# Kernel tuning notes

Measured on AMD Instinct MI355X. Metric: run time of the kernel, lower is better.

## Reference

```python
import jax, jax.numpy as jnp
import numpy as np

N = 50000        # total nodes (disjoint batch of graphs)
E = 800000       # total edges
F_IN = 8         # node feature dim
S = 6            # edge feature dim
H = 20           # ECC kernel-network hidden size (hidden_states)
N_OUT = 20       # ECC output channels (n_out=hidden_states)
G = 32           # GCN channels
D1 = 16          # first dense
N_GRAPHS = 512   # graphs in batch


def setup_inputs() -> dict:
    key = jax.random.key(0)
    ks = jax.random.split(key, 24)
    r = lambda k, sh, s: jax.random.normal(k, sh, dtype=jnp.float32) * s
    return {
        "x": r(ks[0], (N, F_IN), 1.0),
        "e": r(ks[1], (E, S), 1.0),
        "edge_index": jax.random.randint(ks[2], (2, E), 0, N, dtype=jnp.int32),
        "seg": jnp.sort(jax.random.randint(ks[3], (N,), 0, N_GRAPHS, dtype=jnp.int32)),
        # ECC kernel network: S -> H -> H -> F_IN*N_OUT
        "ecc_w1": r(ks[4], (S, H), 0.4), "ecc_b1": jnp.zeros((H,), jnp.float32),
        "ecc_w2": r(ks[5], (H, H), 0.2), "ecc_b2": jnp.zeros((H,), jnp.float32),
        "ecc_w3": r(ks[6], (H, F_IN * N_OUT), 0.2), "ecc_b3": jnp.zeros((F_IN * N_OUT,), jnp.float32),
        "ecc_root": r(ks[7], (F_IN, N_OUT), 0.3), "ecc_b": jnp.zeros((N_OUT,), jnp.float32),
        "gcn1_w": r(ks[8], (N_OUT, G), 0.2), "gcn1_b": jnp.zeros((G,), jnp.float32),
        "gcn2_w": r(ks[9], (G, G), 0.2), "gcn2_b": jnp.zeros((G,), jnp.float32),
        "d1_w": r(ks[10], (G, D1), 0.2), "d1_b": jnp.zeros((D1,), jnp.float32),
        "d2_w": r(ks[11], (D1, 1), 0.2), "d2_b": jnp.zeros((1,), jnp.float32),
    }


def reference(x, e, edge_index, seg,
              ecc_w1, ecc_b1, ecc_w2, ecc_b2, ecc_w3, ecc_b3, ecc_root, ecc_b,
              gcn1_w, gcn1_b, gcn2_w, gcn2_b, d1_w, d1_b, d2_w, d2_b):
    row, col = edge_index[0], edge_index[1]  # message col -> row

    # --- ECCConv: per-edge MLP produces an [F_IN, N_OUT] filter per edge ---
    h = jax.nn.relu(e @ ecc_w1 + ecc_b1)
    h = jax.nn.relu(h @ ecc_w2 + ecc_b2)
    w_edge = (h @ ecc_w3 + ecc_b3).reshape(E, F_IN, N_OUT)   # [E, F_in, F_out]
    msg = jnp.einsum('ef,efo->eo', x[col], w_edge)            # per-edge message
    agg = jax.ops.segment_sum(msg, row, num_segments=N)
    x1 = jax.nn.relu(agg + x @ ecc_root + ecc_b)              # root + bias + relu

    # --- GCN normalization from the edge list (A + I, symmetric norm) ---
    deg = jax.ops.segment_sum(jnp.ones((E,), x.dtype), row, num_segments=N) + 1.0
    dinv = jax.lax.rsqrt(deg)
    edge_norm = (dinv[row] * dinv[col])[:, None]
    self_norm = (dinv * dinv)[:, None]

    def gcn(hin, W, b):
        hw = hin @ W
        nmsg = jax.ops.segment_sum(edge_norm * hw[col], row, num_segments=N)
        return jax.nn.relu(nmsg + self_norm * hw + b)

    x2 = gcn(x1, gcn1_w, gcn1_b)
    x3 = gcn(x2, gcn2_w, gcn2_b)

    # --- GlobalSumPool over graph ids, then MLP head ---
    pooled = jax.ops.segment_sum(x3, seg, num_segments=N_GRAPHS)  # [n_graphs, G]
    out = (pooled @ d1_w + d1_b) @ d2_w + d2_b                    # [n_graphs, 1]
    return out
```

## Files before the change

kernel.cpp:

```cpp
#include <hip/hip_runtime.h>
#include <hip/hip_bf16.h>

#define S_DIM   6
#define H_DIM   20
#define F_INN   8
#define N_OUTC  20
#define G_DIM   32
#define D1_DIM  16
#define NGRAPH  512
#define CAP     32

typedef short short8 __attribute__((ext_vector_type(8)));
typedef float floatx4 __attribute__((ext_vector_type(4)));

__device__ __forceinline__ unsigned short f2bf(float f) {
    unsigned u = __float_as_uint(f);
    return (unsigned short)((u + 0x8000u) >> 16);
}
__device__ __forceinline__ float bf2f(unsigned short s) {
    return __uint_as_float(((unsigned)s) << 16);
}
__device__ __forceinline__ unsigned pk2bf(float a, float b) {
    union { __hip_bfloat162 b2; unsigned u; } cv;
    cv.b2 = __float22bfloat162_rn(make_float2(a, b));
    return cv.u;
}

__global__ __launch_bounds__(256) void loc_kernel(
    const int* __restrict__ ei, int E, int* __restrict__ cnt,
    int* __restrict__ loc,
    const float* __restrict__ w3, const float* __restrict__ b3,
    unsigned short* __restrict__ B3f)
{
    int i = blockIdx.x * 256 + threadIdx.x;
    if (i < 6144) {
        int jj   = i & 7;
        int n    = (i >> 3) & 15;
        int quad = (i >> 7) & 3;
        int nt   = (i >> 9) & 1;
        int s    = i >> 10;
        int K = 32 * s + quad * 8 + jj;
        int o = n + 16 * nt;
        float v = 0.0f;
        if (o < N_OUTC) {
            if (K < 160)      v = w3[(K >> 3) * 160 + (K & 7) * N_OUTC + o];
            else if (K < 168) v = b3[(K - 160) * N_OUTC + o];
        }
        B3f[i] = f2bf(v);
    }
    if (i >= E) return;
    loc[i] = atomicAdd(&cnt[ei[i]], 1);
}

__global__ __launch_bounds__(256) void scanA_kernel(
    const int* __restrict__ deg, int N, int* __restrict__ bsum)
{
    int i = blockIdx.x * 256 + threadIdx.x;
    int v = (i < N) ? deg[i] : 0;
#pragma unroll
    for (int d = 1; d < 64; d <<= 1) v += __shfl_down(v, d, 64);
    __shared__ int ws[4];
    int wid = threadIdx.x >> 6;
    if ((threadIdx.x & 63) == 0) ws[wid] = v;
    __syncthreads();
    if (threadIdx.x == 0) bsum[blockIdx.x] = ws[0] + ws[1] + ws[2] + ws[3];
}

__global__ __launch_bounds__(256) void scanC_kernel(
    const int* __restrict__ deg, int N, const int* __restrict__ bsum, int nbl,
    int E, int* __restrict__ rowptr, float* __restrict__ dinv)
{
    __shared__ int ws[4];
    __shared__ int sboff;
    int t = threadIdx.x;
    {
        int v = (t < nbl && t < blockIdx.x) ? bsum[t] : 0;
#pragma unroll
        for (int d = 1; d < 64; d <<= 1) v += __shfl_down(v, d, 64);
        int wid = t >> 6;
        if ((t & 63) == 0) ws[wid] = v;
        __syncthreads();
        if (t == 0) sboff = ws[0] + ws[1] + ws[2] + ws[3];
        __syncthreads();
    }

    int i = blockIdx.x * 256 + t;
    int d0 = (i < N) ? deg[i] : 0;
    int v = d0;
#pragma unroll
    for (int d = 1; d < 64; d <<= 1) {
        int u = __shfl_up(v, d, 64);
        if ((t & 63) >= d) v += u;
    }
    __shared__ int ws2[4];
    int wid = t >> 6;
    if ((t & 63) == 63) ws2[wid] = v;
    __syncthreads();
    int woff = 0;
    for (int w = 0; w < wid; ++w) woff += ws2[w];
    if (i < N) {
        rowptr[i] = sboff + woff + v - d0;
        dinv[i] = rsqrtf((float)d0 + 1.0f);
    }
    if (blockIdx.x == 0 && t == 0) rowptr[N] = E;
}

__global__ __launch_bounds__(256) void build_kernel(
    const int* __restrict__ ei, int E, const float* __restrict__ e,
    const int* __restrict__ rowptr, const int* __restrict__ loc,
    int4* __restrict__ e_sorted)
{
    int i = blockIdx.x * 256 + threadIdx.x;
    if (i >= E) return;
    int r = ei[i];
    int c = ei[E + i];
    int p = rowptr[r] + loc[i];

    const float2* ep = (const float2*)&e[(size_t)i * S_DIM];
    float2 e0 = ep[0], e1 = ep[1], e2 = ep[2];

    int4 rec;
    rec.x = c;
    rec.y = (int)pk2bf(e0.x, e0.y);
    rec.z = (int)pk2bf(e1.x, e1.y);
    rec.w = (int)pk2bf(e2.x, e2.y);
    e_sorted[p] = rec;
}

__global__ __launch_bounds__(256) void ecc_mfma_kernel(
    const int4* __restrict__ e_sorted, const float* __restrict__ x,
    const int* __restrict__ rowptr, int N, int E,
    const unsigned short* __restrict__ B3f,
    const float* __restrict__ w1, const float* __restrict__ b1,
    const float* __restrict__ w2, const float* __restrict__ b2,
    const float* __restrict__ root, const float* __restrict__ eb,
    const float* __restrict__ g1w,
    float* __restrict__ agg, int* __restrict__ col_sorted,
    unsigned short* __restrict__ hws1)
{
    __shared__ char smem[20480];
    __shared__ float x1buf[CAP * N_OUTC];
    __shared__ int rbounds[2];
    unsigned short (*h2b)[N_OUTC] = (unsigned short (*)[N_OUTC])smem;
    unsigned short (*xb)[F_INN]   = (unsigned short (*)[F_INN])(smem + 10240);
    float* lmsg = (float*)smem;

    int t = threadIdx.x;
    int j0 = blockIdx.x * 256;
    int jend = min(j0 + 256, E);
    int j = j0 + t;

    if (t < 2) {
        int s = (t == 0) ? j0 : (jend - 1);
        int lo = 0, hi = N - 1;
        while (lo < hi) {
            int m = (lo + hi + 1) >> 1;
            if (rowptr[m] <= s) lo = m; else hi = m - 1;
        }
        rbounds[t] = lo;
    }

    if (j < E) {
        int4 rec = e_sorted[j];
        int c = rec.x;
        col_sorted[j] = c;
        float ef[S_DIM] = {
            bf2f((unsigned short)(rec.y & 0xffff)),
            bf2f((unsigned short)((unsigned)rec.y >> 16)),
            bf2f((unsigned short)(rec.z & 0xffff)),
            bf2f((unsigned short)((unsigned)rec.z >> 16)),
            bf2f((unsigned short)(rec.w & 0xffff)),
            bf2f((unsigned short)((unsigned)rec.w >> 16))
        };

        float h1[H_DIM];
#pragma unroll
        for (int jj = 0; jj < H_DIM; ++jj) {
            float a = b1[jj];
#pragma unroll
            for (int s = 0; s < S_DIM; ++s) a = fmaf(ef[s], w1[s * H_DIM + jj], a);
            h1[jj] = fmaxf(a, 0.0f);
        }

        float h2[H_DIM];
#pragma unroll
        for (int jj = 0; jj < H_DIM; ++jj) {
            float a = b2[jj];
#pragma unroll
            for (int k = 0; k < H_DIM; ++k) a = fmaf(h1[k], w2[k * H_DIM + jj], a);
            h2[jj] = fmaxf(a, 0.0f);
        }

        const float4* xp = (const float4*)&x[(size_t)c * F_INN];
        float4 xa = xp[0], xb4 = xp[1];
        float xf[F_INN] = {xa.x, xa.y, xa.z, xa.w, xb4.x, xb4.y, xb4.z, xb4.w};

#pragma unroll
        for (int p = 0; p < N_OUTC / 2; ++p)
            *(unsigned*)&h2b[t][2 * p] = pk2bf(h2[2 * p], h2[2 * p + 1]);
#pragma unroll
        for (int p = 0; p < F_INN / 2; ++p)
            *(unsigned*)&xb[t][2 * p] = pk2bf(xf[2 * p], xf[2 * p + 1]);
    } else {
#pragma unroll
        for (int p = 0; p < N_OUTC / 2; ++p) *(unsigned*)&h2b[t][2 * p] = 0u;
#pragma unroll
        for (int p = 0; p < F_INN / 2; ++p)  *(unsigned*)&xb[t][2 * p] = 0u;
    }
    __syncthreads();

    int lane = t & 63;
    int quad = lane >> 4;
    int n = lane & 15;
    const short8* Bg = (const short8*)B3f;
    short8 Bf[12];
#pragma unroll
    for (int s = 0; s < 6; ++s)
#pragma unroll
        for (int nt = 0; nt < 2; ++nt)
            Bf[s * 2 + nt] = Bg[((s * 2 + nt) * 4 + quad) * 16 + n];

    int w = t >> 6;
    floatx4 acc0s[4], acc1s[4];
#pragma unroll
    for (int T = 0; T < 4; ++T) {
        int base = w * 64 + T * 16;
        int m = base + n;

        const short8 xv8 = *(const short8*)&xb[m][0];
        float xfl[F_INN];
#pragma unroll
        for (int jj = 0; jj < F_INN; ++jj) xfl[jj] = bf2f((unsigned short)xv8[jj]);

        floatx4 acc0 = {0.f, 0.f, 0.f, 0.f};
        floatx4 acc1 = {0.f, 0.f, 0.f, 0.f};
#pragma unroll
        for (int s = 0; s < 6; ++s) {
            short8 A = {0, 0, 0, 0, 0, 0, 0, 0};
            if (s < 5) {
                float h = bf2f(h2b[m][4 * s + quad]);
                union { short8 s8; unsigned u[4]; } av;
#pragma unroll
                for (int p = 0; p < 4; ++p)
                    av.u[p] = pk2bf(h * xfl[2 * p], h * xfl[2 * p + 1]);
                A = av.s8;
            } else if (quad == 0) {
                A = xv8;
            }
            acc0 = __builtin_amdgcn_mfma_f32_16x16x32_bf16(A, Bf[s * 2 + 0], acc0, 0, 0, 0);
            acc1 = __builtin_amdgcn_mfma_f32_16x16x32_bf16(A, Bf[s * 2 + 1], acc1, 0, 0, 0);
        }
        acc0s[T] = acc0;
        acc1s[T] = acc1;
    }
    __syncthreads();

#pragma unroll
    for (int T = 0; T < 4; ++T) {
        int base = w * 64 + T * 16;
#pragma unroll
        for (int r = 0; r < 4; ++r) {
            int row = base + quad * 4 + r;
            lmsg[row * N_OUTC + n] = acc0s[T][r];
            if (n < 4) lmsg[row * N_OUTC + 16 + n] = acc1s[T][r];
        }
    }
    __syncthreads();

    int r0 = rbounds[0], r1 = rbounds[1];
    int nrows = r1 - r0 + 1;
    int work = nrows * 5;
    for (int ww = t; ww < work; ww += 256) {
        int idx = ww / 5;
        int q = ww - idx * 5;
        int row = r0 + idx;
        int a0 = rowptr[row], a1 = rowptr[row + 1];
        int s0 = max(a0, j0), s1 = min(a1, jend);
        float ac0 = 0.f, ac1 = 0.f, ac2 = 0.f, ac3 = 0.f;
        for (int s = s0; s < s1; ++s) {
            const float4 v = *(const float4*)&lmsg[(s - j0) * N_OUTC + q * 4];
            ac0 += v.x; ac1 += v.y; ac2 += v.z; ac3 += v.w;
        }
        bool owned = (a0 >= j0 && a1 <= jend);
        if (owned && idx < CAP) {
            const float4* xp = (const float4*)&x[(size_t)row * F_INN];
            float4 xa = xp[0], xb4 = xp[1];
            float rx[F_INN] = {xa.x, xa.y, xa.z, xa.w, xb4.x, xb4.y, xb4.z, xb4.w};
            float av[4] = {ac0, ac1, ac2, ac3};
#pragma unroll
            for (int u = 0; u < 4; ++u) {
                int oc = q * 4 + u;
                float a = av[u] + eb[oc];
#pragma unroll
                for (int f = 0; f < F_INN; ++f)
                    a = fmaf(rx[f], root[f * N_OUTC + oc], a);
                x1buf[idx * N_OUTC + oc] = fmaxf(a, 0.0f);
            }
        } else {
            float* dst = &agg[(size_t)row * N_OUTC + q * 4];
            if (owned) {
                *(float4*)dst = make_float4(ac0, ac1, ac2, ac3);
            } else {
                unsafeAtomicAdd(dst + 0, ac0);
                unsafeAtomicAdd(dst + 1, ac1);
                unsafeAtomicAdd(dst + 2, ac2);
                unsafeAtomicAdd(dst + 3, ac3);
            }
        }
    }
    __syncthreads();

    int fast = min(nrows, CAP);
    int work2 = fast * 8;
    for (int ww = t; ww < work2; ww += 256) {
        int idx = ww >> 3;
        int qc = ww & 7;
        int row = r0 + idx;
        int a0 = rowptr[row], a1 = rowptr[row + 1];
        if (!(a0 >= j0 && a1 <= jend)) continue;
        float di = rsqrtf((float)(a1 - a0) + 1.0f);
        float m0 = 0.f, m1 = 0.f, m2 = 0.f, m3 = 0.f;
        const float* xr = &x1buf[idx * N_OUTC];
#pragma unroll
        for (int o = 0; o < N_OUTC; ++o) {
            float xv = xr[o];
            const float4 g = *(const float4*)&g1w[o * G_DIM + qc * 4];
            m0 = fmaf(xv, g.x, m0); m1 = fmaf(xv, g.y, m1);
            m2 = fmaf(xv, g.z, m2); m3 = fmaf(xv, g.w, m3);
        }
        unsigned lo32 = pk2bf(m0 * di, m1 * di);
        unsigned hi32 = pk2bf(m2 * di, m3 * di);
        *(uint2*)&hws1[(size_t)row * G_DIM + qc * 4] = make_uint2(lo32, hi32);
    }
}

__global__ __launch_bounds__(256) void cleanup_kernel(
    const float* __restrict__ agg, const float* __restrict__ x,
    const int* __restrict__ rowptr, int N,
    const float* __restrict__ root, const float* __restrict__ eb,
    const float* __restrict__ g1w,
    unsigned short* __restrict__ hws1)
{
    int n = blockIdx.x * 256 + threadIdx.x;
    if (n >= N) return;
    int a0 = rowptr[n], a1 = rowptr[n + 1];
    bool contained = (a1 > a0) ? ((a0 >> 8) == ((a1 - 1) >> 8))
                               : ((a0 & 255) != 0);
    if (contained) {
        int target = (a0 >> 8) << 8;
        int lo = 0, hi = N - 1;
        while (lo < hi) {
            int m = (lo + hi + 1) >> 1;
            if (rowptr[m] <= target) lo = m; else hi = m - 1;
        }
        if (n - lo < CAP) return;
    }

    const float4* xp = (const float4*)&x[(size_t)n * F_INN];
    float4 xa = xp[0], xb = xp[1];
    float xf[F_INN] = {xa.x, xa.y, xa.z, xa.w, xb.x, xb.y, xb.z, xb.w};

    float x1[N_OUTC];
#pragma unroll
    for (int o = 0; o < N_OUTC; ++o) {
        float a = agg[(size_t)n * N_OUTC + o] + eb[o];
#pragma unroll
        for (int f = 0; f < F_INN; ++f) a = fmaf(xf[f], root[f * N_OUTC + o], a);
        x1[o] = fmaxf(a, 0.0f);
    }

    float di = rsqrtf((float)(a1 - a0) + 1.0f);
#pragma unroll
    for (int q = 0; q < 4; ++q) {
        float a[8];
#pragma unroll
        for (int u = 0; u < 8; ++u) {
            int g = q * 8 + u;
            float acc = 0.0f;
#pragma unroll
            for (int o = 0; o < N_OUTC; ++o) acc = fmaf(x1[o], g1w[o * G_DIM + g], acc);
            a[u] = acc * di;
        }
        union { short8 s8; unsigned u4[4]; } ov;
#pragma unroll
        for (int p = 0; p < 4; ++p) ov.u4[p] = pk2bf(a[2 * p], a[2 * p + 1]);
        *(short8*)&hws1[(size_t)n * G_DIM + q * 8] = ov.s8;
    }
}

template<bool DO_MATMUL>
__global__ __launch_bounds__(256) void gcn_gather_kernel(
    const unsigned short* __restrict__ hws, const int* __restrict__ rowptr,
    const int* __restrict__ col_sorted, const float* __restrict__ dinv, int N,
    const float* __restrict__ bias, const float* __restrict__ w2,
    unsigned short* __restrict__ outbuf)
{
    __shared__ float x2s[DO_MATMUL ? 64 * 33 : 1];
    __shared__ float w2s[DO_MATMUL ? G_DIM * G_DIM : 1];

    int t = threadIdx.x;
    int nl = t >> 2;
    int q = t & 3;
    int n = blockIdx.x * 64 + nl;

    if (DO_MATMUL) {
        ((float4*)w2s)[t] = ((const float4*)w2)[t];
        __syncthreads();
    }

    float xo[8];
    float di = 0.0f;
    if (n < N) {
        di = dinv[n];
        int j0 = rowptr[n], j1 = rowptr[n + 1];
        short8 sv = *(const short8*)&hws[(size_t)n * G_DIM + q * 8];
        float s[8];
#pragma unroll
        for (int k = 0; k < 8; ++k) s[k] = bf2f((unsigned short)sv[k]);
        int j = j0;
        for (; j + 4 <= j1; j += 4) {
            int c0 = col_sorted[j + 0];
            int c1 = col_sorted[j + 1];
            int c2 = col_sorted[j + 2];
            int c3 = col_sorted[j + 3];
            short8 v0 = *(const short8*)&hws[(size_t)c0 * G_DIM + q * 8];
            short8 v1 = *(const short8*)&hws[(size_t)c1 * G_DIM + q * 8];
            short8 v2 = *(const short8*)&hws[(size_t)c2 * G_DIM + q * 8];
            short8 v3 = *(const short8*)&hws[(size_t)c3 * G_DIM + q * 8];
#pragma unroll
            for (int k = 0; k < 8; ++k)
                s[k] += (bf2f((unsigned short)v0[k]) + bf2f((unsigned short)v1[k]))
                      + (bf2f((unsigned short)v2[k]) + bf2f((unsigned short)v3[k]));
        }
        for (; j < j1; ++j) {
            int c = col_sorted[j];
            short8 v = *(const short8*)&hws[(size_t)c * G_DIM + q * 8];
#pragma unroll
            for (int k = 0; k < 8; ++k) s[k] += bf2f((unsigned short)v[k]);
        }
#pragma unroll
        for (int k = 0; k < 8; ++k)
            xo[k] = fmaxf(fmaf(di, s[k], bias[q * 8 + k]), 0.0f);
    } else {
#pragma unroll
        for (int k = 0; k < 8; ++k) xo[k] = 0.0f;
    }

    if (DO_MATMUL) {
#pragma unroll
        for (int k = 0; k < 8; ++k) x2s[nl * 33 + q * 8 + k] = xo[k];
        __syncthreads();
        if (n < N) {
            float a[8];
#pragma unroll
            for (int k = 0; k < 8; ++k) a[k] = 0.0f;
#pragma unroll
            for (int g = 0; g < G_DIM; ++g) {
                float xv = x2s[nl * 33 + g];
#pragma unroll
                for (int k = 0; k < 8; ++k)
                    a[k] = fmaf(xv, w2s[g * G_DIM + q * 8 + k], a[k]);
            }
            union { short8 s8; unsigned u4[4]; } ov;
#pragma unroll
            for (int p = 0; p < 4; ++p) ov.u4[p] = pk2bf(a[2 * p] * di, a[2 * p + 1] * di);
            *(short8*)&outbuf[(size_t)n * G_DIM + q * 8] = ov.s8;
        }
    } else {
        if (n < N) {
            union { short8 s8; unsigned u4[4]; } ov;
#pragma unroll
            for (int p = 0; p < 4; ++p) ov.u4[p] = pk2bf(xo[2 * p], xo[2 * p + 1]);
            *(short8*)&outbuf[(size_t)n * G_DIM + q * 8] = ov.s8;
        }
    }
}

__global__ __launch_bounds__(256) void pool_head_kernel(
    const unsigned short* __restrict__ x3, const int* __restrict__ seg, int N,
    const float* __restrict__ d1w, const float* __restrict__ d1b,
    const float* __restrict__ d2w, const float* __restrict__ d2b,
    float* __restrict__ out)
{
    __shared__ float red[8][G_DIM];
    __shared__ float pvec[G_DIM];
    __shared__ int bounds[2];
    int g = blockIdx.x;
    int t = threadIdx.x;
    if (t < 2) {
        int target = g + t;
        int lo = 0, hi = N;
        while (lo < hi) {
            int m = (lo + hi) >> 1;
            if (seg[m] < target) lo = m + 1; else hi = m;
        }
        bounds[t] = lo;
    }
    __syncthreads();
    int n0 = bounds[0], n1 = bounds[1];
    int ch = t & (G_DIM - 1);
    int slice = t >> 5;
    float a = 0.0f;
    for (int n = n0 + slice; n < n1; n += 8)
        a += bf2f(x3[(size_t)n * G_DIM + ch]);
    red[slice][ch] = a;
    __syncthreads();
    if (slice == 0) {
        float s = red[0][ch];
#pragma unroll
        for (int k = 1; k < 8; ++k) s += red[k][ch];
        pvec[ch] = s;
    }
    __syncthreads();
    if (t < 64) {
        float acc = 0.0f;
        if (t < D1_DIM) {
            float tj = d1b[t];
#pragma unroll
            for (int gg = 0; gg < G_DIM; ++gg)
                tj = fmaf(pvec[gg], d1w[gg * D1_DIM + t], tj);
            acc = tj * d2w[t];
        }
#pragma unroll
        for (int d = 1; d < D1_DIM; d <<= 1) acc += __shfl_down(acc, d, 64);
        if (t == 0) out[g] = acc + d2b[0];
    }
}

extern "C" void kernel_launch(void* const* d_in, const int* in_sizes, int n_in,
                              void* d_out, int out_size, void* d_ws, size_t ws_size,
                              hipStream_t stream)
{
    const float* x    = (const float*)d_in[0];
    const float* e    = (const float*)d_in[1];
    const int*   ei   = (const int*)d_in[2];
    const int*   seg  = (const int*)d_in[3];
    const float* w1   = (const float*)d_in[4];
    const float* b1   = (const float*)d_in[5];
    const float* w2   = (const float*)d_in[6];
    const float* b2   = (const float*)d_in[7];
    const float* w3   = (const float*)d_in[8];
    const float* b3   = (const float*)d_in[9];
    const float* root = (const float*)d_in[10];
    const float* eb   = (const float*)d_in[11];
    const float* g1w  = (const float*)d_in[12];
    const float* g1b  = (const float*)d_in[13];
    const float* g2w  = (const float*)d_in[14];
    const float* g2b  = (const float*)d_in[15];
    const float* d1w  = (const float*)d_in[16];
    const float* d1b  = (const float*)d_in[17];
    const float* d2w  = (const float*)d_in[18];
    const float* d2b  = (const float*)d_in[19];

    const int N = in_sizes[3];
    const int E = in_sizes[1] / S_DIM;
    float* out = (float*)d_out;

    const int nbl = (N + 255) / 256;
    const int ebl = (E + 255) / 256;

    char* ws = (char*)d_ws;
    size_t off = 0;
    auto alloc = [&](size_t elems) -> char* {
        char* p = ws + off;
        off += ((elems * 4 + 15) & ~(size_t)15);
        return p;
    };
    int*   cnt        = (int*)  alloc(N);
    float* agg        = (float*)alloc((size_t)N * N_OUTC);
    size_t zero_bytes = off;
    int*   rowptr     = (int*)  alloc(N + 1);
    int*   bsum       = (int*)  alloc(nbl);
    float* dinv       = (float*)alloc(N);
    int*   loc        = (int*)  alloc(E);
    int*   col_sorted = (int*)  alloc(E);
    unsigned short* B3f = (unsigned short*)alloc(6144 / 2);
    int4*  e_sorted   = (int4*) alloc((size_t)E * 4);
    unsigned short* hws1 = (unsigned short*)alloc((size_t)N * G_DIM / 2);
    unsigned short* hws2 = (unsigned short*)alloc((size_t)N * G_DIM / 2);
    unsigned short* x3   = (unsigned short*)alloc((size_t)N * G_DIM / 2);
    (void)ws_size;

    hipMemsetAsync(d_ws, 0, zero_bytes, stream);

    loc_kernel<<<ebl, 256, 0, stream>>>(ei, E, cnt, loc, w3, b3, B3f);
    scanA_kernel<<<nbl, 256, 0, stream>>>(cnt, N, bsum);
    scanC_kernel<<<nbl, 256, 0, stream>>>(cnt, N, bsum, nbl, E, rowptr, dinv);
    build_kernel<<<ebl, 256, 0, stream>>>(ei, E, e, rowptr, loc, e_sorted);
    ecc_mfma_kernel<<<ebl, 256, 0, stream>>>(e_sorted, x, rowptr, N, E, B3f,
                                             w1, b1, w2, b2, root, eb, g1w,
                                             agg, col_sorted, hws1);
    cleanup_kernel<<<nbl, 256, 0, stream>>>(agg, x, rowptr, N, root, eb, g1w, hws1);
    gcn_gather_kernel<true><<<(N + 63) / 64, 256, 0, stream>>>(
        hws1, rowptr, col_sorted, dinv, N, g1b, g2w, hws2);
    gcn_gather_kernel<false><<<(N + 63) / 64, 256, 0, stream>>>(
        hws2, rowptr, col_sorted, dinv, N, g2b, nullptr, x3);
    pool_head_kernel<<<NGRAPH, 256, 0, stream>>>(x3, seg, N, d1w, d1b, d2w, d2b, out);
}
```

Measured before the change: 262.6 us.

## Move edge MLP into build kernel and split GCN gather into 8 lanes per node

After: 273.8 us. +4.3%, slower.

```diff
diff --git a/kernel.cpp b/kernel.cpp
--- a/kernel.cpp
+++ b/kernel.cpp
@@ -108,6 +108,8 @@
 __global__ __launch_bounds__(256) void build_kernel(
     const int* __restrict__ ei, int E, const float* __restrict__ e,
     const int* __restrict__ rowptr, const int* __restrict__ loc,
+    const float* __restrict__ w1, const float* __restrict__ b1,
+    const float* __restrict__ w2, const float* __restrict__ b2,
     int4* __restrict__ e_sorted)
 {
     int i = blockIdx.x * 256 + threadIdx.x;
@@ -118,21 +120,50 @@
 
     const float2* ep = (const float2*)&e[(size_t)i * S_DIM];
     float2 e0 = ep[0], e1 = ep[1], e2 = ep[2];
-
-    int4 rec;
-    rec.x = c;
-    rec.y = (int)pk2bf(e0.x, e0.y);
-    rec.z = (int)pk2bf(e1.x, e1.y);
-    rec.w = (int)pk2bf(e2.x, e2.y);
-    e_sorted[p] = rec;
+    float ef[S_DIM] = {e0.x, e0.y, e1.x, e1.y, e2.x, e2.y};
+
+    float h1[H_DIM];
+#pragma unroll
+    for (int jj = 0; jj < H_DIM; ++jj) {
+        float a = b1[jj];
+#pragma unroll
+        for (int s = 0; s < S_DIM; ++s) a = fmaf(ef[s], w1[s * H_DIM + jj], a);
+        h1[jj] = fmaxf(a, 0.0f);
+    }
+
+    float h2[H_DIM];
+#pragma unroll
+    for (int jj = 0; jj < H_DIM; ++jj) {
+        float a = b2[jj];
+#pragma unroll
+        for (int k = 0; k < H_DIM; ++k) a = fmaf(h1[k], w2[k * H_DIM + jj], a);
+        h2[jj] = fmaxf(a, 0.0f);
+    }
+
+    int4 r0, r1, r2;
+    r0.x = c;
+    r0.y = (int)pk2bf(h2[0],  h2[1]);
+    r0.z = (int)pk2bf(h2[2],  h2[3]);
+    r0.w = (int)pk2bf(h2[4],  h2[5]);
+    r1.x = (int)pk2bf(h2[6],  h2[7]);
+    r1.y = (int)pk2bf(h2[8],  h2[9]);
+    r1.z = (int)pk2bf(h2[10], h2[11]);
+    r1.w = (int)pk2bf(h2[12], h2[13]);
+    r2.x = (int)pk2bf(h2[14], h2[15]);
+    r2.y = (int)pk2bf(h2[16], h2[17]);
+    r2.z = (int)pk2bf(h2[18], h2[19]);
+    r2.w = 0;
+
+    int4* dst = &e_sorted[(size_t)p * 3];
+    dst[0] = r0;
+    dst[1] = r1;
+    dst[2] = r2;
 }
 
 __global__ __launch_bounds__(256) void ecc_mfma_kernel(
     const int4* __restrict__ e_sorted, const float* __restrict__ x,
     const int* __restrict__ rowptr, int N, int E,
     const unsigned short* __restrict__ B3f,
-    const float* __restrict__ w1, const float* __restrict__ b1,
-    const float* __restrict__ w2, const float* __restrict__ b2,
     const float* __restrict__ root, const float* __restrict__ eb,
     const float* __restrict__ g1w,
     float* __restrict__ agg, int* __restrict__ col_sorted,
@@ -161,51 +192,32 @@
     }
 
     if (j < E) {
-        int4 rec = e_sorted[j];
-        int c = rec.x;
+        const int4* er = &e_sorted[(size_t)j * 3];
+        int4 r0 = er[0];
+        int4 r1 = er[1];
+        int4 r2 = er[2];
+        int c = r0.x;
         col_sorted[j] = c;
-        float ef[S_DIM] = {
-            bf2f((unsigned short)(rec.y & 0xffff)),
-            bf2f((unsigned short)((unsigned)rec.y >> 16)),
-            bf2f((unsigned short)(rec.z & 0xffff)),
-            bf2f((unsigned short)((unsigned)rec.z >> 16)),
-            bf2f((unsigned short)(rec.w & 0xffff)),
-            bf2f((unsigned short)((unsigned)rec.w >> 16))
-        };
-
-        float h1[H_DIM];
-#pragma unroll
-        for (int jj = 0; jj < H_DIM; ++jj) {
-            float a = b1[jj];
-#pragma unroll
-            for (int s = 0; s < S_DIM; ++s) a = fmaf(ef[s], w1[s * H_DIM + jj], a);
-            h1[jj] = fmaxf(a, 0.0f);
-        }
-
-        float h2[H_DIM];
-#pragma unroll
-        for (int jj = 0; jj < H_DIM; ++jj) {
-            float a = b2[jj];
-#pragma unroll
-            for (int k = 0; k < H_DIM; ++k) a = fmaf(h1[k], w2[k * H_DIM + jj], a);
-            h2[jj] = fmaxf(a, 0.0f);
-        }
+
+        uint2* hdst = (uint2*)&h2b[t][0];
+        hdst[0] = make_uint2((unsigned)r0.y, (unsigned)r0.z);
+        hdst[1] = make_uint2((unsigned)r0.w, (unsigned)r1.x);
+        hdst[2] = make_uint2((unsigned)r1.y, (unsigned)r1.z);
+        hdst[3] = make_uint2((unsigned)r1.w, (unsigned)r2.x);
+        hdst[4] = make_uint2((unsigned)r2.y, (unsigned)r2.z);
 
         const float4* xp = (const float4*)&x[(size_t)c * F_INN];
         float4 xa = xp[0], xb4 = xp[1];
         float xf[F_INN] = {xa.x, xa.y, xa.z, xa.w, xb4.x, xb4.y, xb4.z, xb4.w};
-
-#pragma unroll
-        for (int p = 0; p < N_OUTC / 2; ++p)
-            *(unsigned*)&h2b[t][2 * p] = pk2bf(h2[2 * p], h2[2 * p + 1]);
 #pragma unroll
         for (int p = 0; p < F_INN / 2; ++p)
             *(unsigned*)&xb[t][2 * p] = pk2bf(xf[2 * p], xf[2 * p + 1]);
     } else {
-#pragma unroll
-        for (int p = 0; p < N_OUTC / 2; ++p) *(unsigned*)&h2b[t][2 * p] = 0u;
-#pragma unroll
-        for (int p = 0; p < F_INN / 2; ++p)  *(unsigned*)&xb[t][2 * p] = 0u;
+        uint2* hdst = (uint2*)&h2b[t][0];
+#pragma unroll
+        for (int p = 0; p < 5; ++p) hdst[p] = make_uint2(0u, 0u);
+#pragma unroll
+        for (int p = 0; p < F_INN / 2; ++p) *(unsigned*)&xb[t][2 * p] = 0u;
     }
     __syncthreads();
 
@@ -267,13 +279,13 @@
     }
     __syncthreads();
 
-    int r0 = rbounds[0], r1 = rbounds[1];
-    int nrows = r1 - r0 + 1;
+    int r0_ = rbounds[0], r1_ = rbounds[1];
+    int nrows = r1_ - r0_ + 1;
     int work = nrows * 5;
     for (int ww = t; ww < work; ww += 256) {
         int idx = ww / 5;
         int q = ww - idx * 5;
-        int row = r0 + idx;
+        int row = r0_ + idx;
         int a0 = rowptr[row], a1 = rowptr[row + 1];
         int s0 = max(a0, j0), s1 = min(a1, jend);
         float ac0 = 0.f, ac1 = 0.f, ac2 = 0.f, ac3 = 0.f;
@@ -315,7 +327,7 @@
     for (int ww = t; ww < work2; ww += 256) {
         int idx = ww >> 3;
         int qc = ww & 7;
-        int row = r0 + idx;
+        int row = r0_ + idx;
         int a0 = rowptr[row], a1 = rowptr[row + 1];
         if (!(a0 >= j0 && a1 <= jend)) continue;
         float di = rsqrtf((float)(a1 - a0) + 1.0f);
@@ -395,83 +407,86 @@
     const float* __restrict__ bias, const float* __restrict__ w2,
     unsigned short* __restrict__ outbuf)
 {
-    __shared__ float x2s[DO_MATMUL ? 64 * 33 : 1];
+    __shared__ float x2s[DO_MATMUL ? 32 * 33 : 1];
     __shared__ float w2s[DO_MATMUL ? G_DIM * G_DIM : 1];
 
     int t = threadIdx.x;
-    int nl = t >> 2;
-    int q = t & 3;
-    int n = blockIdx.x * 64 + nl;
+    int nl = t >> 3;
+    int q = t & 7;
+    int n = blockIdx.x * 32 + nl;
 
     if (DO_MATMUL) {
         ((float4*)w2s)[t] = ((const float4*)w2)[t];
         __syncthreads();
     }
 
-    float xo[8];
+    float xo[4];
     float di = 0.0f;
     if (n < N) {
         di = dinv[n];
         int j0 = rowptr[n], j1 = rowptr[n + 1];
-        short8 sv = *(const short8*)&hws[(size_t)n * G_DIM + q * 8];
-        float s[8];
-#pragma unroll
-        for (int k = 0; k < 8; ++k) s[k] = bf2f((unsigned short)sv[k]);
+        uint2 sv = *(const uint2*)&hws[(size_t)n * G_DIM + q * 4];
+        float s[4];
+        s[0] = bf2f((unsigned short)(sv.x & 0xffff));
+        s[1] = bf2f((unsigned short)(sv.x >> 16));
+        s[2] = bf2f((unsigned short)(sv.y & 0xffff));
+        s[3] = bf2f((unsigned short)(sv.y >> 16));
         int j = j0;
         for (; j + 4 <= j1; j += 4) {
             int c0 = col_sorted[j + 0];
             int c1 = col_sorted[j + 1];
             int c2 = col_sorted[j + 2];
             int c3 = col_sorted[j + 3];
-            short8 v0 = *(const short8*)&hws[(size_t)c0 * G_DIM + q * 8];
-            short8 v1 = *(const short8*)&hws[(size_t)c1 * G_DIM + q * 8];
-            short8 v2 = *(const short8*)&hws[(size_t)c2 * G_DIM + q * 8];
-            short8 v3 = *(const short8*)&hws[(size_t)c3 * G_DIM + q * 8];
-#pragma unroll
-            for (int k = 0; k < 8; ++k)
-                s[k] += (bf2f((unsigned short)v0[k]) + bf2f((unsigned short)v1[k]))
-                      + (bf2f((unsigned short)v2[k]) + bf2f((unsigned short)v3[k]));
+            uint2 v0 = *(const uint2*)&hws[(size_t)c0 * G_DIM + q * 4];
+            uint2 v1 = *(const uint2*)&hws[(size_t)c1 * G_DIM + q * 4];
+            uint2 v2 = *(const uint2*)&hws[(size_t)c2 * G_DIM + q * 4];
+            uint2 v3 = *(const uint2*)&hws[(size_t)c3 * G_DIM + q * 4];
+            s[0] += (bf2f((unsigned short)(v0.x & 0xffff)) + bf2f((unsigned short)(v1.x & 0xffff)))
+                  + (bf2f((unsigned short)(v2.x & 0xffff)) + bf2f((unsigned short)(v3.x & 0xffff)));
+            s[1] += (bf2f((unsigned short)(v0.x >> 16)) + bf2f((unsigned short)(v1.x >> 16)))
+                  + (bf2f((unsigned short)(v2.x >> 16)) + bf2f((unsigned short)(v3.x >> 16)));
+            s[2] += (bf2f((unsigned short)(v0.y & 0xffff)) + bf2f((unsigned short)(v1.y & 0xffff)))
+                  + (bf2f((unsigned short)(v2.y & 0xffff)) + bf2f((unsigned short)(v3.y & 0xffff)));
+            s[3] += (bf2f((unsigned short)(v0.y >> 16)) + bf2f((unsigned short)(v1.y >> 16)))
+                  + (bf2f((unsigned short)(v2.y >> 16)) + bf2f((unsigned short)(v3.y >> 16)));
         }
         for (; j < j1; ++j) {
             int c = col_sorted[j];
-            short8 v = *(const short8*)&hws[(size_t)c * G_DIM + q * 8];
-#pragma unroll
-            for (int k = 0; k < 8; ++k) s[k] += bf2f((unsigned short)v[k]);
-        }
-#pragma unroll
-        for (int k = 0; k < 8; ++k)
-            xo[k] = fmaxf(fmaf(di, s[k], bias[q * 8 + k]), 0.0f);
+            uint2 v = *(const uint2*)&hws[(size_t)c * G_DIM + q * 4];
+            s[0] += bf2f((unsigned short)(v.x & 0xffff));
+            s[1] += bf2f((unsigned short)(v.x >> 16));
+            s[2] += bf2f((unsigned short)(v.y & 0xffff));
+            s[3] += bf2f((unsigned short)(v.y >> 16));
+        }
+#pragma unroll
+        for (int k = 0; k < 4; ++k)
+            xo[k] = fmaxf(fmaf(di, s[k], bias[q * 4 + k]), 0.0f);
     } else {
 #pragma unroll
-        for (int k = 0; k < 8; ++k) xo[k] = 0.0f;
+        for (int k = 0; k < 4; ++k) xo[k] = 0.0f;
     }
 
     if (DO_MATMUL) {
 #pragma unroll
-        for (int k = 0; k < 8; ++k) x2s[nl * 33 + q * 8 + k] = xo[k];
+        for (int k = 0; k < 4; ++k) x2s[nl * 33 + q * 4 + k] = xo[k];
         __syncthreads();
         if (n < N) {
-            float a[8];
-#pragma unroll
-            for (int k = 0; k < 8; ++k) a[k] = 0.0f;
+            float a[4] = {0.f, 0.f, 0.f, 0.f};
 #pragma unroll
             for (int g = 0; g < G_DIM; ++g) {
                 float xv = x2s[nl * 33 + g];
 #pragma unroll
-                for (int k = 0; k < 8; ++k)
-                    a[k] = fmaf(xv, w2s[g * G_DIM + q * 8 + k], a[k]);
+                for (int k = 0; k < 4; ++k)
+                    a[k] = fmaf(xv, w2s[g * G_DIM + q * 4 + k], a[k]);
             }
-            union { short8 s8; unsigned u4[4]; } ov;
-#pragma unroll
-            for (int p = 0; p < 4; ++p) ov.u4[p] = pk2bf(a[2 * p] * di, a[2 * p + 1] * di);
-            *(short8*)&outbuf[(size_t)n * G_DIM + q * 8] = ov.s8;
+            uint2 ov = make_uint2(pk2bf(a[0] * di, a[1] * di),
+                                  pk2bf(a[2] * di, a[3] * di));
+            *(uint2*)&outbuf[(size_t)n * G_DIM + q * 4] = ov;
         }
     } else {
         if (n < N) {
-            union { short8 s8; unsigned u4[4]; } ov;
-#pragma unroll
-            for (int p = 0; p < 4; ++p) ov.u4[p] = pk2bf(xo[2 * p], xo[2 * p + 1]);
-            *(short8*)&outbuf[(size_t)n * G_DIM + q * 8] = ov.s8;
+            uint2 ov = make_uint2(pk2bf(xo[0], xo[1]), pk2bf(xo[2], xo[3]));
+            *(uint2*)&outbuf[(size_t)n * G_DIM + q * 4] = ov;
         }
     }
 }
@@ -575,7 +590,7 @@
     int*   loc        = (int*)  alloc(E);
     int*   col_sorted = (int*)  alloc(E);
     unsigned short* B3f = (unsigned short*)alloc(6144 / 2);
-    int4*  e_sorted   = (int4*) alloc((size_t)E * 4);
+    int4*  e_sorted   = (int4*) alloc((size_t)E * 12);
     unsigned short* hws1 = (unsigned short*)alloc((size_t)N * G_DIM / 2);
     unsigned short* hws2 = (unsigned short*)alloc((size_t)N * G_DIM / 2);
     unsigned short* x3   = (unsigned short*)alloc((size_t)N * G_DIM / 2);
@@ -586,14 +601,15 @@
     loc_kernel<<<ebl, 256, 0, stream>>>(ei, E, cnt, loc, w3, b3, B3f);
     scanA_kernel<<<nbl, 256, 0, stream>>>(cnt, N, bsum);
     scanC_kernel<<<nbl, 256, 0, stream>>>(cnt, N, bsum, nbl, E, rowptr, dinv);
-    build_kernel<<<ebl, 256, 0, stream>>>(ei, E, e, rowptr, loc, e_sorted);
+    build_kernel<<<ebl, 256, 0, stream>>>(ei, E, e, rowptr, loc,
+                                          w1, b1, w2, b2, e_sorted);
     ecc_mfma_kernel<<<ebl, 256, 0, stream>>>(e_sorted, x, rowptr, N, E, B3f,
-                                             w1, b1, w2, b2, root, eb, g1w,
+                                             root, eb, g1w,
                                              agg, col_sorted, hws1);
     cleanup_kernel<<<nbl, 256, 0, stream>>>(agg, x, rowptr, N, root, eb, g1w, hws1);
-    gcn_gather_kernel<true><<<(N + 63) / 64, 256, 0, stream>>>(
+    gcn_gather_kernel<true><<<(N + 31) / 32, 256, 0, stream>>>(
         hws1, rowptr, col_sorted, dinv, N, g1b, g2w, hws2);
-    gcn_gather_kernel<false><<<(N + 63) / 64, 256, 0, stream>>>(
+    gcn_gather_kernel<false><<<(N + 31) / 32, 256, 0, stream>>>(
         hws2, rowptr, col_sorted, dinv, N, g2b, nullptr, x3);
     pool_head_kernel<<<NGRAPH, 256, 0, stream>>>(x3, seg, N, d1w, d1b, d2w, d2b, out);
 }
```
